# Optimization experiments

Hardware: AMD Instinct MI355X
Metric: run time of the kernel (lower is better)

The kernel has to match this reference:

```python
import jax, jax.numpy as jnp
import numpy as np

N, E = 10000, 320000
IN_F, OUT_F = 512, 256
ALPHA = 0.2  # leaky_relu negative slope
NEG_BIG = -9e15


def setup_inputs() -> dict:
    key = jax.random.key(0)
    k1, k2, k3, k4 = jax.random.split(key, 4)
    x = jax.random.normal(k1, (N, IN_F), dtype=jnp.float32)
    # fc: Linear(in_features, out_features) -> W [out, in], b [out] (init to 0 per reset_parameters)
    W = jax.random.normal(k2, (OUT_F, IN_F), dtype=jnp.float32) * (1.414 / np.sqrt(IN_F))
    b = jnp.zeros((OUT_F,), dtype=jnp.float32)
    # att: Conv1d(1,1,2*out) == dot with vector a [2*out]
    a = jax.random.normal(k3, (2 * OUT_F,), dtype=jnp.float32) * (1.414 / np.sqrt(2 * OUT_F))
    edge_list = jax.random.randint(k4, (2, E), 0, N, dtype=jnp.int64)
    return {"x": x, "W": W, "b": b, "a": a, "edge_list": edge_list}


def reference(x, W, b, a, edge_list):
    # eval mode: dropout is identity
    src, tgt = edge_list[0], edge_list[1]
    h = x @ W.T + b  # [N, out]
    out_f = h.shape[1]
    # conv1d over concatenated [h_src, h_tgt] with kernel length 2*out == split dot product
    score = h[src] @ a[:out_f] + h[tgt] @ a[out_f:]  # [E]
    score = jax.nn.leaky_relu(score, negative_slope=ALPHA)
    n = x.shape[0]
    # torch.sparse.FloatTensor(...).to_dense() sums duplicate edges -> scatter-add
    adj = jnp.zeros((n, n), dtype=h.dtype).at[src, tgt].add(score)
    adj = jnp.where(adj == 0, jnp.asarray(NEG_BIG, h.dtype), adj)
    adj = jax.nn.softmax(adj, axis=1)
    return adj @ h  # [N, out]
```

## Files before the change

kernel.cpp:

```cpp
#include <hip/hip_runtime.h>
#include <hip/hip_bf16.h>
#include <math.h>

#define IN_F 512
#define OUT_F 256
#define ALPHA 0.2f
#define CAP 512
#define NCHAIN 16

typedef __attribute__((ext_vector_type(8))) short bf16x8;
typedef __attribute__((ext_vector_type(4))) float f32x4;

static __device__ __forceinline__ unsigned short f2bf(float f) {
  unsigned int u = __builtin_bit_cast(unsigned int, f);
  return (unsigned short)((u + 0x8000u) >> 16);
}
static __device__ __forceinline__ float bf_lo(unsigned int u) {
  return __builtin_bit_cast(float, u << 16);
}
static __device__ __forceinline__ float bf_hi(unsigned int u) {
  return __builtin_bit_cast(float, u & 0xffff0000u);
}

__global__ __launch_bounds__(256) void mega(const float* __restrict__ x,
                                            const float* __restrict__ W,
                                            const float* __restrict__ bias,
                                            const float* __restrict__ a,
                                            const int* __restrict__ edges,
                                            unsigned short* __restrict__ hb,
                                            float* __restrict__ s1p,
                                            float* __restrict__ s2p,
                                            float* __restrict__ hsump,
                                            int* __restrict__ head,
                                            int2* __restrict__ rec,
                                            int N_, int E_, int m32, int gblocks) {
  const int tid = threadIdx.x;
  const int vb = blockIdx.x;

  if (vb >= gblocks) {
    int idx = (vb - gblocks) * 256 + tid;
    if (idx < E_) {
      int srcv = edges[idx];
      int tgtv = edges[E_ + idx];
      int old = atomicExch(&head[srcv * NCHAIN + (idx & (NCHAIN - 1))], idx);
      rec[idx] = make_int2(old, tgtv);
    }
    return;
  }

  __shared__ unsigned short lA[32][136];
  __shared__ unsigned short lB[64][136];
  __shared__ float s1t[32], s2t[32], ht[64];

  const int mt = vb % m32;
  const int bn4 = vb / m32;
  const int bm = mt * 32;
  const int bn = bn4 * 64;
  const int wave = tid >> 6, lane = tid & 63;
  const int lr = lane & 15, lk = lane >> 4;

  f32x4 acc[2] = {};

  for (int k0 = 0; k0 < IN_F; k0 += 128) {
#pragma unroll
    for (int r = 0; r < 4; ++r) {
      int idx = tid + r * 256;
      int row = idx >> 5, c4 = idx & 31;
      int gm = bm + row;
      float4 va = (gm < N_) ? *(const float4*)&x[(size_t)gm * IN_F + k0 + c4 * 4]
                            : make_float4(0.f, 0.f, 0.f, 0.f);
      ushort4 oa;
      oa.x = f2bf(va.x); oa.y = f2bf(va.y); oa.z = f2bf(va.z); oa.w = f2bf(va.w);
      *(ushort4*)&lA[row][c4 * 4] = oa;
    }
#pragma unroll
    for (int r = 0; r < 8; ++r) {
      int idx = tid + r * 256;
      int row = idx >> 5, c4 = idx & 31;
      float4 vb4 = *(const float4*)&W[(size_t)(bn + row) * IN_F + k0 + c4 * 4];
      ushort4 ob;
      ob.x = f2bf(vb4.x); ob.y = f2bf(vb4.y); ob.z = f2bf(vb4.z); ob.w = f2bf(vb4.w);
      *(ushort4*)&lB[row][c4 * 4] = ob;
    }
    __syncthreads();
#pragma unroll
    for (int kk = 0; kk < 128; kk += 32) {
      bf16x8 af[2], bfr;
#pragma unroll
      for (int fm = 0; fm < 2; ++fm)
        af[fm] = *(const bf16x8*)&lA[fm * 16 + lr][kk + lk * 8];
      bfr = *(const bf16x8*)&lB[wave * 16 + lr][kk + lk * 8];
#pragma unroll
      for (int fm = 0; fm < 2; ++fm)
        acc[fm] = __builtin_amdgcn_mfma_f32_16x16x32_bf16(af[fm], bfr, acc[fm], 0, 0, 0);
    }
    __syncthreads();
  }

  if (tid < 32) { s1t[tid] = 0.f; s2t[tid] = 0.f; }
  __syncthreads();

  const int gcv = bn + wave * 16 + lr;
  const float av = a[gcv], bv2 = a[OUT_F + gcv], biasv = bias[gcv];
  float csum = 0.f;
#pragma unroll
  for (int fm = 0; fm < 2; ++fm) {
#pragma unroll
    for (int i = 0; i < 4; ++i) {
      int lrow = fm * 16 + lk * 4 + i;
      int gr = bm + lrow;
      bool valid = (gr < N_);
      float v = valid ? acc[fm][i] + biasv : 0.f;
      if (valid) hb[(size_t)gr * OUT_F + gcv] = f2bf(v);
      csum += v;
      float p1 = v * av;
      float p2 = v * bv2;
#pragma unroll
      for (int off = 1; off < 16; off <<= 1) {
        p1 += __shfl_xor(p1, off);
        p2 += __shfl_xor(p2, off);
      }
      if (lr == 0 && valid) {
        atomicAdd(&s1t[lrow], p1);
        atomicAdd(&s2t[lrow], p2);
      }
    }
  }
#pragma unroll
  for (int off = 16; off < 64; off <<= 1) csum += __shfl_xor(csum, off);
  if (lk == 0) ht[wave * 16 + lr] = csum;
  __syncthreads();

  if (tid < 32) {
    int gr = bm + tid;
    if (gr < N_) {
      s1p[(size_t)gr * 4 + bn4] = s1t[tid];
      s2p[(size_t)gr * 4 + bn4] = s2t[tid];
    }
  }
  if (tid < 64) hsump[(size_t)mt * OUT_F + bn + tid] = ht[tid];
}

__global__ __launch_bounds__(128) void rowk(const unsigned short* __restrict__ hb,
                                            const float* __restrict__ s1p,
                                            const float* __restrict__ s2p,
                                            const float* __restrict__ hsump,
                                            int* __restrict__ head,
                                            const int2* __restrict__ rec,
                                            float* __restrict__ out,
                                            int N_, int E_, int m32) {
  __shared__ int s_tgt[CAP];
  __shared__ float s_w[CAP];
  __shared__ float s_acc[4][OUT_F];
  __shared__ float s_red[4];
  __shared__ int s_cnt;

  const int t = threadIdx.x;
  const int lane = t & 63, wv = t >> 6;
  const int row = blockIdx.x;
  const float invN = 1.0f / (float)N_;

  if (t == 0) s_cnt = 0;
  __syncthreads();

  if (t < NCHAIN) {
    int e = head[row * NCHAIN + t];
    int guard = 0;
    while (e >= 0 && e < E_ && guard < CAP) {
      int2 rr = rec[e];
      int slot = atomicAdd(&s_cnt, 1);
      if (slot < CAP) s_tgt[slot] = rr.y;
      ++guard;
      e = rr.x;
    }
    head[row * NCHAIN + t] = -1;
  }
  __syncthreads();
  int deg = s_cnt;
  if (deg > CAP) deg = CAP;

  float4 sv = *(const float4*)&s1p[(size_t)row * 4];
  float s1i = (sv.x + sv.y) + (sv.z + sv.w);
  for (int q = t; q < deg; q += 128) {
    int tg = s_tgt[q];
    float4 s2v = *(const float4*)&s2p[(size_t)tg * 4];
    float s = s1i + ((s2v.x + s2v.y) + (s2v.z + s2v.w));
    s_w[q] = (s > 0.f) ? s : ALPHA * s;
  }
  __syncthreads();

  for (int q = t; q < deg; q += 128) {
    int tg = s_tgt[q];
    int first = q, cnt = 0;
    for (int j = 0; j < deg; ++j) {
      int tj = s_tgt[j];
      cnt += (tj == tg);
      if (tj == tg && j < first) first = j;
    }
    float v;
    if (first == q) {
      v = (float)cnt * s_w[q];
      if (v == 0.f) v = -INFINITY;
    } else {
      v = -INFINITY;
    }
    s_w[q] = v;
  }

  float m = -INFINITY;
  for (int q = t; q < deg; q += 128) m = fmaxf(m, s_w[q]);
#pragma unroll
  for (int off = 32; off; off >>= 1) m = fmaxf(m, __shfl_xor(m, off));
  if (lane == 0) s_red[wv] = m;
  __syncthreads();
  m = fmaxf(s_red[0], s_red[1]);

  bool uniform = (deg == 0) || (m == -INFINITY);

  float dsum = 0.f;
  if (!uniform) {
    for (int q = t; q < deg; q += 128) {
      float e = __expf(s_w[q] - m);
      s_w[q] = e;
      dsum += e;
    }
  }
#pragma unroll
  for (int off = 32; off; off >>= 1) dsum += __shfl_xor(dsum, off);
  if (lane == 0) s_red[2 + wv] = dsum;
  __syncthreads();
  float inv = 1.0f / (s_red[2] + s_red[3]);

  float2* out2 = (float2*)(out + (size_t)row * OUT_F);
  if (uniform) {
    float A = 0.f, B = 0.f;
    for (int mt = 0; mt < m32; ++mt) {
      A += hsump[(size_t)mt * OUT_F + 2 * t];
      B += hsump[(size_t)mt * OUT_F + 2 * t + 1];
    }
    out2[t] = make_float2(A * invN, B * invN);
    return;
  }

  const int g = t >> 5, lane32 = t & 31;
  float a0 = 0.f, a1 = 0.f, a2 = 0.f, a3 = 0.f, a4 = 0.f, a5 = 0.f, a6 = 0.f, a7 = 0.f;
  const uint4* hb4 = (const uint4*)hb;
#pragma unroll 2
  for (int q = g; q < deg; q += 4) {
    float w = s_w[q];
    uint4 u = hb4[(size_t)s_tgt[q] * 32 + lane32];
    a0 += w * bf_lo(u.x); a1 += w * bf_hi(u.x);
    a2 += w * bf_lo(u.y); a3 += w * bf_hi(u.y);
    a4 += w * bf_lo(u.z); a5 += w * bf_hi(u.z);
    a6 += w * bf_lo(u.w); a7 += w * bf_hi(u.w);
  }
  {
    float* dst = &s_acc[g][lane32 * 8];
    dst[0] = a0; dst[1] = a1; dst[2] = a2; dst[3] = a3;
    dst[4] = a4; dst[5] = a5; dst[6] = a6; dst[7] = a7;
  }
  __syncthreads();
  float A = ((s_acc[0][2 * t] + s_acc[1][2 * t]) + (s_acc[2][2 * t] + s_acc[3][2 * t]));
  float B = ((s_acc[0][2 * t + 1] + s_acc[1][2 * t + 1]) +
             (s_acc[2][2 * t + 1] + s_acc[3][2 * t + 1]));
  out2[t] = make_float2(A * inv, B * inv);
}

extern "C" void kernel_launch(void* const* d_in, const int* in_sizes, int n_in,
                              void* d_out, int out_size, void* d_ws, size_t ws_size,
                              hipStream_t stream) {
  const float* x = (const float*)d_in[0];
  const float* W = (const float*)d_in[1];
  const float* b = (const float*)d_in[2];
  const float* a = (const float*)d_in[3];
  const int* edges = (const int*)d_in[4];
  float* out = (float*)d_out;

  int N_ = in_sizes[0] / IN_F;
  int E_ = in_sizes[4] / 2;

  char* ws = (char*)d_ws;
  size_t off = 0;
  auto alloc = [&](size_t bytes) {
    char* q = ws + off;
    off = (off + bytes + 255) & ~(size_t)255;
    return q;
  };
  int m32 = (N_ + 31) / 32;
  unsigned short* hb    = (unsigned short*)alloc((size_t)N_ * OUT_F * sizeof(unsigned short));
  float*          s1p   = (float*)alloc((size_t)N_ * 4 * sizeof(float));
  float*          s2p   = (float*)alloc((size_t)N_ * 4 * sizeof(float));
  float*          hsump = (float*)alloc((size_t)m32 * OUT_F * sizeof(float));
  int*            head  = (int*)alloc((size_t)NCHAIN * N_ * sizeof(int));
  int2*           rec   = (int2*)alloc((size_t)E_ * sizeof(int2));

  int gblocks = m32 * 4;
  int fblocks = (E_ + 255) / 256;

  mega<<<gblocks + fblocks, 256, 0, stream>>>(x, W, b, a, edges, hb, s1p, s2p, hsump,
                                              head, rec, N_, E_, m32, gblocks);
  rowk<<<N_, 128, 0, stream>>>(hb, s1p, s2p, hsump, head, rec, out, N_, E_, m32);
}
```

Before: 62.73 us.

## Load GEMM fragments directly from global memory, bypassing LDS staging

The projection GEMM stops staging x and W tiles through shared memory with barriers. Each lane now loads its MFMA fragment straight from global memory, packs it to bf16 in registers, and the k-loop is unrolled. This removes the LDS round trip and the __syncthreads stalls. In exchange, each x row is read by all four waves and each W row by many blocks through cache, and the per-lane loads are strided rows rather than coalesced. Rows past N are clamped to the last row instead of being zeroed, which relies on the later store guard to discard them.

```diff
diff --git a/kernel.cpp b/kernel.cpp
--- a/kernel.cpp
+++ b/kernel.cpp
@@ -11,6 +11,17 @@
 typedef __attribute__((ext_vector_type(8))) short bf16x8;
 typedef __attribute__((ext_vector_type(4))) float f32x4;
 
+static __device__ __forceinline__ unsigned int pk2(float a, float b) {
+  unsigned int ua = __builtin_bit_cast(unsigned int, a) + 0x8000u;
+  unsigned int ub = __builtin_bit_cast(unsigned int, b) + 0x8000u;
+  return (ua >> 16) | (ub & 0xffff0000u);
+}
+static __device__ __forceinline__ bf16x8 pack8(float4 lo, float4 hi) {
+  union { unsigned int u[4]; bf16x8 v; } r;
+  r.u[0] = pk2(lo.x, lo.y); r.u[1] = pk2(lo.z, lo.w);
+  r.u[2] = pk2(hi.x, hi.y); r.u[3] = pk2(hi.z, hi.w);
+  return r.v;
+}
 static __device__ __forceinline__ unsigned short f2bf(float f) {
   unsigned int u = __builtin_bit_cast(unsigned int, f);
   return (unsigned short)((u + 0x8000u) >> 16);
@@ -48,8 +59,6 @@
     return;
   }
 
-  __shared__ unsigned short lA[32][136];
-  __shared__ unsigned short lB[64][136];
   __shared__ float s1t[32], s2t[32], ht[64];
 
   const int mt = vb % m32;
@@ -59,42 +68,26 @@
   const int wave = tid >> 6, lane = tid & 63;
   const int lr = lane & 15, lk = lane >> 4;
 
+  int gr0 = bm + lr;        if (gr0 >= N_) gr0 = N_ - 1;
+  int gr1 = bm + 16 + lr;   if (gr1 >= N_) gr1 = N_ - 1;
+  const float* xr0 = x + (size_t)gr0 * IN_F;
+  const float* xr1 = x + (size_t)gr1 * IN_F;
+  const float* wr  = W + (size_t)(bn + wave * 16 + lr) * IN_F;
+
   f32x4 acc[2] = {};
 
-  for (int k0 = 0; k0 < IN_F; k0 += 128) {
-#pragma unroll
-    for (int r = 0; r < 4; ++r) {
-      int idx = tid + r * 256;
-      int row = idx >> 5, c4 = idx & 31;
-      int gm = bm + row;
-      float4 va = (gm < N_) ? *(const float4*)&x[(size_t)gm * IN_F + k0 + c4 * 4]
-                            : make_float4(0.f, 0.f, 0.f, 0.f);
-      ushort4 oa;
-      oa.x = f2bf(va.x); oa.y = f2bf(va.y); oa.z = f2bf(va.z); oa.w = f2bf(va.w);
-      *(ushort4*)&lA[row][c4 * 4] = oa;
-    }
-#pragma unroll
-    for (int r = 0; r < 8; ++r) {
-      int idx = tid + r * 256;
-      int row = idx >> 5, c4 = idx & 31;
-      float4 vb4 = *(const float4*)&W[(size_t)(bn + row) * IN_F + k0 + c4 * 4];
-      ushort4 ob;
-      ob.x = f2bf(vb4.x); ob.y = f2bf(vb4.y); ob.z = f2bf(vb4.z); ob.w = f2bf(vb4.w);
-      *(ushort4*)&lB[row][c4 * 4] = ob;
-    }
-    __syncthreads();
-#pragma unroll
-    for (int kk = 0; kk < 128; kk += 32) {
-      bf16x8 af[2], bfr;
-#pragma unroll
-      for (int fm = 0; fm < 2; ++fm)
-        af[fm] = *(const bf16x8*)&lA[fm * 16 + lr][kk + lk * 8];
-      bfr = *(const bf16x8*)&lB[wave * 16 + lr][kk + lk * 8];
-#pragma unroll
-      for (int fm = 0; fm < 2; ++fm)
-        acc[fm] = __builtin_amdgcn_mfma_f32_16x16x32_bf16(af[fm], bfr, acc[fm], 0, 0, 0);
-    }
-    __syncthreads();
+#pragma unroll 4
+  for (int kk = 0; kk < IN_F; kk += 32) {
+    const int kb = kk + lk * 8;
+    float4 a0 = *(const float4*)&xr0[kb];
+    float4 a1 = *(const float4*)&xr0[kb + 4];
+    float4 c0 = *(const float4*)&xr1[kb];
+    float4 c1 = *(const float4*)&xr1[kb + 4];
+    float4 b0 = *(const float4*)&wr[kb];
+    float4 b1 = *(const float4*)&wr[kb + 4];
+    bf16x8 fb = pack8(b0, b1);
+    acc[0] = __builtin_amdgcn_mfma_f32_16x16x32_bf16(pack8(a0, a1), fb, acc[0], 0, 0, 0);
+    acc[1] = __builtin_amdgcn_mfma_f32_16x16x32_bf16(pack8(c0, c1), fb, acc[1], 0, 0, 0);
   }
 
   if (tid < 32) { s1t[tid] = 0.f; s2t[tid] = 0.f; }
```

Result: slower. 115.6 us (+84.2%).
